# Optimization experiments

Hardware: AMD Instinct MI355X
Metric: run time of the kernel (lower is better)

## Reference

```python
import jax, jax.numpy as jnp
import numpy as np

NUM_USERS = 100000
NUM_ITEMS = 50000
HIDDEN = 64
NUM_LAYERS = 3
NUM_EDGES = 1200000
N = NUM_USERS + NUM_ITEMS


def setup_inputs() -> dict:
    key = jax.random.key(0)
    k_e, k_u, k_i, k_w, k_b = jax.random.split(key, 5)
    edge_index = jax.random.randint(k_e, (2, NUM_EDGES), 0, N, dtype=jnp.int32)
    users_emb = jax.random.normal(k_u, (NUM_USERS, HIDDEN), dtype=jnp.float32) * 0.01
    items_emb = jax.random.normal(k_i, (NUM_ITEMS, HIDDEN), dtype=jnp.float32) * 0.01
    # GCNConv linear weights (glorot-ish) and zero biases, stacked over layers
    scale = 1.0 / np.sqrt(HIDDEN)
    Ws = jax.random.uniform(k_w, (NUM_LAYERS, HIDDEN, HIDDEN), dtype=jnp.float32,
                            minval=-scale, maxval=scale)
    bs = jnp.zeros((NUM_LAYERS, HIDDEN), dtype=jnp.float32)
    return {"edge_index": edge_index, "users_emb": users_emb,
            "items_emb": items_emb, "Ws": Ws, "bs": bs}


def reference(edge_index, users_emb, items_emb, Ws, bs):
    # GraphSAGEModel.forward: concat user/item embeddings, run num_layers GCNConv
    # (PyG defaults: add self-loops, symmetric D^-1/2 A D^-1/2 normalization, bias).
    x = jnp.concatenate([users_emb, items_emb], axis=0)  # [N, H]

    self_loops = jnp.arange(N, dtype=edge_index.dtype)
    src = jnp.concatenate([edge_index[0], self_loops])  # [E+N]
    dst = jnp.concatenate([edge_index[1], self_loops])

    ones = jnp.ones(src.shape[0], dtype=x.dtype)
    deg = jax.ops.segment_sum(ones, dst, num_segments=N)  # in-degree incl self loop
    dinv = jnp.where(deg > 0, jax.lax.rsqrt(deg), 0.0)
    norm = dinv[src] * dinv[dst]  # [E+N], graph-constant across layers

    for l in range(NUM_LAYERS):
        h = x @ Ws[l]                       # linear transform [N, H]
        msg = h[src] * norm[:, None]        # gather + scale
        x = jax.ops.segment_sum(msg, dst, num_segments=N) + bs[l]
    return (x[:NUM_USERS], users_emb, x[NUM_USERS:], items_emb)
```

## Files before the change

### kernel.cpp

```cpp
#include <hip/hip_runtime.h>
#include <hip/hip_fp16.h>

#define NU 100000
#define NI 50000
#define NN 150000
#define HH 64
#define NE 1200000

#define SCAN_CHUNK 1024
#define NBLK ((NN + SCAN_CHUNK - 1) / SCAN_CHUNK)
#define AGG_BLOCKS (NN / 8)

__global__ __launch_bounds__(256) void k_rank(const int4* __restrict__ dst4,
                                              int* __restrict__ counts,
                                              int4* __restrict__ rank4,
                                              __half* __restrict__ pad0,
                                              __half* __restrict__ pad1,
                                              float* __restrict__ dinv,
                                              float* __restrict__ p1u) {
    if (blockIdx.x == 0 && threadIdx.x < 18) {
        if (threadIdx.x < 8)       ((int4*)pad0)[threadIdx.x] = make_int4(0, 0, 0, 0);
        else if (threadIdx.x < 16) ((int4*)pad1)[threadIdx.x - 8] = make_int4(0, 0, 0, 0);
        else if (threadIdx.x == 16) dinv[NN] = 0.f;
        else                        p1u[NN] = 0.f;
    }
    int t = blockIdx.x * blockDim.x + threadIdx.x;
    if (t >= NE / 8) return;
    int4 d0 = dst4[2 * t], d1 = dst4[2 * t + 1];
    int4 r0, r1;
    r0.x = atomicAdd(&counts[d0.x], 1);
    r0.y = atomicAdd(&counts[d0.y], 1);
    r0.z = atomicAdd(&counts[d0.z], 1);
    r0.w = atomicAdd(&counts[d0.w], 1);
    r1.x = atomicAdd(&counts[d1.x], 1);
    r1.y = atomicAdd(&counts[d1.y], 1);
    r1.z = atomicAdd(&counts[d1.z], 1);
    r1.w = atomicAdd(&counts[d1.w], 1);
    rank4[2 * t]     = r0;
    rank4[2 * t + 1] = r1;
}

__global__ __launch_bounds__(256) void k_scan(const int* __restrict__ counts,
                                              float* __restrict__ dinv,
                                              float* __restrict__ dinv2,
                                              int* __restrict__ row_ptr,
                                              unsigned int* __restrict__ state,
                                              const float* __restrict__ Wfull,
                                              const float* __restrict__ bfull,
                                              float* __restrict__ What,
                                              float* __restrict__ cvec) {
    __shared__ float smem[HH * HH];
    __shared__ int s_prefix;
    int t = threadIdx.x;
    int b = blockIdx.x;

    if (b == NBLK) {
        int r = t >> 2, j0 = (t & 3) * 16;
        const float* W0 = Wfull;
        const float* W1 = Wfull + HH * HH;
        const float* W2 = Wfull + 2 * HH * HH;
        float acc[16];
#pragma unroll
        for (int j = 0; j < 16; ++j) acc[j] = 0.f;
        for (int k = 0; k < HH; ++k) {
            float a = W1[r * HH + k];
            const float* bp = W2 + k * HH + j0;
#pragma unroll
            for (int j = 0; j < 16; ++j) acc[j] += a * bp[j];
        }
#pragma unroll
        for (int j = 0; j < 16; ++j) smem[r * HH + j0 + j] = acc[j];
        if (t < HH) {
            float s = 0.f;
            for (int k = 0; k < HH; ++k) s += bfull[HH + k] * W2[k * HH + t];
            cvec[HH + t] = s;
        }
        __syncthreads();
#pragma unroll
        for (int j = 0; j < 16; ++j) acc[j] = 0.f;
        for (int k = 0; k < HH; ++k) {
            float a = W0[r * HH + k];
            const float* bp = smem + k * HH + j0;
#pragma unroll
            for (int j = 0; j < 16; ++j) acc[j] += a * bp[j];
        }
#pragma unroll
        for (int j = 0; j < 16; ++j) What[r * HH + j0 + j] = acc[j];
        if (t < HH) {
            float s = 0.f;
            for (int k = 0; k < HH; ++k) s += bfull[k] * smem[k * HH + t];
            cvec[t] = s;
        }
        return;
    }

    int* sd = (int*)smem;
    int base = b * SCAN_CHUNK + t * 4;
    int c[4];
    if (base + 3 < NN) {
        int4 v = *(const int4*)(counts + base);
        c[0] = v.x; c[1] = v.y; c[2] = v.z; c[3] = v.w;
    } else {
#pragma unroll
        for (int i = 0; i < 4; ++i) c[i] = (base + i < NN) ? counts[base + i] : 0;
    }
#pragma unroll
    for (int i = 0; i < 4; ++i)
        if (base + i < NN) {
            dinv[base + i]  = rsqrtf((float)(c[i] + 1));
            dinv2[base + i] = 1.0f / (float)(c[i] + 1);
        }

    int tt = c[0] + c[1] + c[2] + c[3];
    sd[t] = tt; __syncthreads();
    for (int off = 1; off < 256; off <<= 1) {
        int x = (t >= off) ? sd[t - off] : 0;
        __syncthreads();
        sd[t] += x;
        __syncthreads();
    }

    if (t == 0) {
        unsigned int agg = (unsigned int)sd[255];
        if (b == 0) {
            __hip_atomic_store(&state[0], (2u << 30) | agg, __ATOMIC_RELEASE,
                               __HIP_MEMORY_SCOPE_AGENT);
            s_prefix = 0;
        } else {
            __hip_atomic_store(&state[b], (1u << 30) | agg, __ATOMIC_RELEASE,
                               __HIP_MEMORY_SCOPE_AGENT);
            unsigned int prefix = 0;
            int p = b - 1;
            while (true) {
                unsigned int s = __hip_atomic_load(&state[p], __ATOMIC_ACQUIRE,
                                                   __HIP_MEMORY_SCOPE_AGENT);
                unsigned int fl = s >> 30;
                if (fl == 0u) { __builtin_amdgcn_s_sleep(1); continue; }
                prefix += s & 0x3FFFFFFFu;
                if (fl == 2u) break;
                --p;
            }
            __hip_atomic_store(&state[b], (2u << 30) | (prefix + agg),
                               __ATOMIC_RELEASE, __HIP_MEMORY_SCOPE_AGENT);
            s_prefix = (int)prefix;
        }
    }
    __syncthreads();

    int off0 = s_prefix + (sd[t] - tt);
    int run = 0;
#pragma unroll
    for (int i = 0; i < 4; ++i) {
        if (base + i < NN) row_ptr[base + i] = off0 + run;
        run += c[i];
    }
    if (b == NBLK - 1 && t == 0) row_ptr[NN] = NE;
}

#define CONCAT_BLOCKS ((NN * 8 + 255) / 256)
#define FILL_BLOCKS   ((NE / 8 + 255) / 256)

__global__ __launch_bounds__(256) void k_concat_fill(
    const float4* __restrict__ users, const float4* __restrict__ items,
    const float* __restrict__ dinv, int4* __restrict__ xs4, float4* __restrict__ out,
    const int4* __restrict__ src4, const int4* __restrict__ dst4,
    const int4* __restrict__ rank4, const int* __restrict__ row_ptr,
    int* __restrict__ col) {
    if (blockIdx.x < CONCAT_BLOCKS) {
        int i = blockIdx.x * 256 + threadIdx.x;
        if (i >= NN * 8) return;
        const int UB8 = NU * 8;
        const int UB4 = NU * 16;
        float4 v0, v1;
        if (i < UB8) {
            v0 = users[2 * i];
            v1 = users[2 * i + 1];
            out[UB4 + 2 * i]     = v0;
            out[UB4 + 2 * i + 1] = v1;
        } else {
            int j = i - UB8;
            v0 = items[2 * j];
            v1 = items[2 * j + 1];
            out[2 * UB4 + NI * 16 + 2 * j]     = v0;
            out[2 * UB4 + NI * 16 + 2 * j + 1] = v1;
        }
        float dv = dinv[i >> 3];
        __half2 h[4];
        h[0] = __halves2half2(__float2half_rn(v0.x * dv), __float2half_rn(v0.y * dv));
        h[1] = __halves2half2(__float2half_rn(v0.z * dv), __float2half_rn(v0.w * dv));
        h[2] = __halves2half2(__float2half_rn(v1.x * dv), __float2half_rn(v1.y * dv));
        h[3] = __halves2half2(__float2half_rn(v1.z * dv), __float2half_rn(v1.w * dv));
        xs4[i] = *(int4*)h;
    } else {
        int t = (blockIdx.x - CONCAT_BLOCKS) * 256 + threadIdx.x;
        if (t >= NE / 8) return;
        int4 s0 = src4[2 * t],  s1 = src4[2 * t + 1];
        int4 d0 = dst4[2 * t],  d1 = dst4[2 * t + 1];
        int4 r0 = rank4[2 * t], r1 = rank4[2 * t + 1];
        int p0 = row_ptr[d0.x], p1 = row_ptr[d0.y], p2 = row_ptr[d0.z], p3 = row_ptr[d0.w];
        int p4 = row_ptr[d1.x], p5 = row_ptr[d1.y], p6 = row_ptr[d1.z], p7 = row_ptr[d1.w];
        col[p0 + r0.x] = s0.x;
        col[p1 + r0.y] = s0.y;
        col[p2 + r0.z] = s0.z;
        col[p3 + r0.w] = s0.w;
        col[p4 + r1.x] = s1.x;
        col[p5 + r1.y] = s1.y;
        col[p6 + r1.z] = s1.z;
        col[p7 + r1.w] = s1.w;
    }
}

template <int UMODE>
__global__ __launch_bounds__(256) void k_aggregate(
    const __half* __restrict__ x, __half* __restrict__ y,
    const float* __restrict__ scale,
    const int* __restrict__ row_ptr, const int* __restrict__ col,
    const float* __restrict__ dinv, const float* __restrict__ pin,
    float* __restrict__ uout, float* __restrict__ pout) {
    int lane = threadIdx.x & 63;
    int wave = blockIdx.x * 4 + (threadIdx.x >> 6);
    int na = wave * 2;
    if (na >= NN) return;
    int nb = na + 1;
    int o  = lane >> 3;
    int f8 = (lane & 7) << 3;

    float a[8], b[8];
#pragma unroll
    for (int j = 0; j < 8; ++j) { a[j] = 0.f; b[j] = 0.f; }
    float ua = 0.f, ub = 0.f;

#define GATHER(r, acc, uacc)                                               \
    {                                                                      \
        int4 raw = *(const int4*)(x + (size_t)(r) * HH + f8);              \
        if (UMODE) uacc += pin[r];                                         \
        __half2* hp = (__half2*)&raw;                                      \
        _Pragma("unroll")                                                  \
        for (int j = 0; j < 4; ++j) {                                      \
            float2 f = __half22float2(hp[j]);                              \
            acc[2 * j] += f.x; acc[2 * j + 1] += f.y;                      \
        }                                                                  \
    }

    int ea = row_ptr[na], enda = row_ptr[na + 1];
    int eb = enda,        endb = row_ptr[nb + 1];

    {
        int ia = ea + o - 1;
        int ib = eb + o - 1;
        int rA = (o == 0) ? na : ((ia < enda) ? col[ia] : NN);
        int rB = (o == 0) ? nb : ((ib < endb) ? col[ib] : NN);
        GATHER(rA, a, ua);
        GATHER(rB, b, ub);
        ea += 7; eb += 7;
    }
    while (ea < enda || eb < endb) {
        int iA = ea + o, iB = eb + o;
        int rA = (iA < enda) ? col[iA] : NN;
        int rB = (iB < endb) ? col[iB] : NN;
        GATHER(rA, a, ua);
        GATHER(rB, b, ub);
        ea += 8; eb += 8;
    }
#undef GATHER

#pragma unroll
    for (int j = 0; j < 8; ++j) {
        a[j] += __shfl_xor(a[j], 8);  b[j] += __shfl_xor(b[j], 8);
        a[j] += __shfl_xor(a[j], 16); b[j] += __shfl_xor(b[j], 16);
        a[j] += __shfl_xor(a[j], 32); b[j] += __shfl_xor(b[j], 32);
    }
    if (UMODE) {
        ua += __shfl_xor(ua, 8);  ub += __shfl_xor(ub, 8);
        ua += __shfl_xor(ua, 16); ub += __shfl_xor(ub, 16);
        ua += __shfl_xor(ua, 32); ub += __shfl_xor(ub, 32);
    }

    if (o < 2) {
        int   n  = (o == 0) ? na : nb;
        float dv = scale[n];
        __half2 h[4];
#pragma unroll
        for (int j = 0; j < 4; ++j) {
            float x0 = (o == 0) ? a[2 * j]     : b[2 * j];
            float x1 = (o == 0) ? a[2 * j + 1] : b[2 * j + 1];
            h[j] = __halves2half2(__float2half_rn(dv * x0), __float2half_rn(dv * x1));
        }
        *(int4*)(y + (size_t)n * HH + f8) = *(int4*)h;
    }
    if (UMODE && lane < 2) {
        int n = na + lane;
        float s = ((lane == 0) ? ua : ub) * 0.125f;
        float dvn = dinv[n];
        float u = dvn * s;
        uout[n] = u;
        if (UMODE == 1) pout[n] = dvn * u;
    }
}

#define GR 128
#define XSS 65
__global__ __launch_bounds__(256) void k_gemm_final(
    const __half* __restrict__ y, const float* __restrict__ W,
    const float* __restrict__ b2, const float* __restrict__ cvec,
    const float* __restrict__ u1, const float* __restrict__ u2,
    float* __restrict__ out_lo, float* __restrict__ out_hi) {
    __shared__ float xs[GR * XSS];
    __shared__ float ws[HH * HH];
    int t = threadIdx.x;
    int rowBase = blockIdx.x * GR;

    {
        const float4* W4 = (const float4*)W;
        float4* ws4 = (float4*)ws;
#pragma unroll
        for (int i = 0; i < 4; ++i) ws4[i * 256 + t] = W4[i * 256 + t];
    }
#pragma unroll
    for (int it = 0; it < 4; ++it) {
        int g = it * 256 + t;
        int r = g >> 3;
        int c0 = (g & 7) * 8;
        int row = rowBase + r;
        if (row < NN) {
            int4 raw = *(const int4*)(y + (size_t)row * HH + c0);
            __half2 h0 = *(__half2*)&raw.x, h1 = *(__half2*)&raw.y;
            __half2 h2 = *(__half2*)&raw.z, h3 = *(__half2*)&raw.w;
            float2 f0 = __half22float2(h0), f1 = __half22float2(h1);
            float2 f2 = __half22float2(h2), f3 = __half22float2(h3);
            float* dp = xs + r * XSS + c0;
            dp[0] = f0.x; dp[1] = f0.y; dp[2] = f1.x; dp[3] = f1.y;
            dp[4] = f2.x; dp[5] = f2.y; dp[6] = f3.x; dp[7] = f3.y;
        }
    }
    __syncthreads();

    int tx = t & 7;
    int ty = t >> 3;
    int j0 = tx * 8;
    int r0 = ty * 4;

    float acc[4][8];
#pragma unroll
    for (int i = 0; i < 4; ++i)
#pragma unroll
        for (int j = 0; j < 8; ++j) acc[i][j] = 0.f;

    for (int k = 0; k < HH; ++k) {
        float4 w0 = *(const float4*)(ws + k * HH + j0);
        float4 w1 = *(const float4*)(ws + k * HH + j0 + 4);
        float wv[8] = {w0.x, w0.y, w0.z, w0.w, w1.x, w1.y, w1.z, w1.w};
#pragma unroll
        for (int i = 0; i < 4; ++i) {
            float xv = xs[(r0 + i) * XSS + k];
#pragma unroll
            for (int j = 0; j < 8; ++j) acc[i][j] += xv * wv[j];
        }
    }

    float c0j[8], c1j[8], b2j[8];
#pragma unroll
    for (int j = 0; j < 8; ++j) {
        c0j[j] = cvec[j0 + j];
        c1j[j] = cvec[HH + j0 + j];
        b2j[j] = b2[j0 + j];
    }

#pragma unroll
    for (int i = 0; i < 4; ++i) {
        int r = rowBase + r0 + i;
        if (r >= NN) continue;
        float u2r = u2[r], u1r = u1[r];
        float base[8];
#pragma unroll
        for (int j = 0; j < 8; ++j) base[j] = u2r * c0j[j] + u1r * c1j[j] + b2j[j];
        float4 o0 = make_float4(acc[i][0] + base[0], acc[i][1] + base[1],
                                acc[i][2] + base[2], acc[i][3] + base[3]);
        float4 o1 = make_float4(acc[i][4] + base[4], acc[i][5] + base[5],
                                acc[i][6] + base[6], acc[i][7] + base[7]);
        float* d = (r < NU) ? (out_lo + (size_t)r * HH)
                            : (out_hi + (size_t)(r - NU) * HH);
        *(float4*)(d + j0) = o0;
        *(float4*)(d + j0 + 4) = o1;
    }
}

extern "C" void kernel_launch(void* const* d_in, const int* in_sizes, int n_in,
                              void* d_out, int out_size, void* d_ws, size_t ws_size,
                              hipStream_t stream) {
    const int*   edge  = (const int*)d_in[0];
    const int*   src   = edge;
    const int*   dst   = edge + NE;
    const float* users = (const float*)d_in[1];
    const float* items = (const float*)d_in[2];
    const float* Ws    = (const float*)d_in[3];
    const float* bs    = (const float*)d_in[4];
    float*       out   = (float*)d_out;

    char* w = (char*)d_ws;
    __half* Xs0     = (__half*)w; w += (size_t)(NN + 1) * HH * 2;
    __half* Xs1     = (__half*)w; w += (size_t)(NN + 1) * HH * 2;
    float*  dinv    = (float*)w;  w += (size_t)(NN + 1) * 4;
    float*  dinv2   = (float*)w;  w += (size_t)NN * 4;
    float*  u1      = (float*)w;  w += (size_t)NN * 4;
    float*  p1u     = (float*)w;  w += (size_t)(NN + 1) * 4;
    float*  u2      = (float*)w;  w += (size_t)NN * 4;
    float*  What    = (float*)w;  w += (size_t)HH * HH * 4;
    float*  cvec    = (float*)w;  w += (size_t)2 * HH * 4;
    unsigned int* state = (unsigned int*)w; w += 256 * 4;
    int*    counts  = (int*)w;    w += (size_t)NN * 4;
    int*    row_ptr = (int*)w;    w += (size_t)(NN + 1) * 4;
    w += 12;
    int*    col     = (int*)w;    w += (size_t)NE * 4;
    int*    rank    = (int*)w;    w += (size_t)NE * 4;
    (void)ws_size; (void)in_sizes; (void)n_in; (void)out_size;

    hipMemsetAsync(state, 0, (size_t)(256 + NN) * sizeof(int), stream);

    k_rank<<<(NE / 8 + 255) / 256, 256, 0, stream>>>(
        (const int4*)dst, counts, (int4*)rank,
        Xs0 + (size_t)NN * HH, Xs1 + (size_t)NN * HH, dinv, p1u);
    k_scan<<<NBLK + 1, 256, 0, stream>>>(counts, dinv, dinv2, row_ptr, state,
                                         Ws, bs, What, cvec);
    k_concat_fill<<<CONCAT_BLOCKS + FILL_BLOCKS, 256, 0, stream>>>(
        (const float4*)users, (const float4*)items, dinv, (int4*)Xs0, (float4*)out,
        (const int4*)src, (const int4*)dst, (const int4*)rank, row_ptr, col);

    k_aggregate<1><<<AGG_BLOCKS, 256, 0, stream>>>(
        Xs0, Xs1, dinv2, row_ptr, col, dinv, dinv, u1, p1u);
    k_aggregate<2><<<AGG_BLOCKS, 256, 0, stream>>>(
        Xs1, Xs0, dinv2, row_ptr, col, dinv, p1u, u2, nullptr);
    k_aggregate<0><<<AGG_BLOCKS, 256, 0, stream>>>(
        Xs0, Xs1, dinv, row_ptr, col, nullptr, nullptr, nullptr, nullptr);

    const int GEMM_BLOCKS = (NN + GR - 1) / GR;
    k_gemm_final<<<GEMM_BLOCKS, 256, 0, stream>>>(
        Xs1, What, bs + 2 * HH, cvec, u1, u2,
        out , out + (size_t)2 * NU * HH );
}
```

Before: 403.9 us.

## Move embedding concat into rank kernel, apply dinv in first aggregate, unroll gather

The fp16 conversion and output copy of the user/item embeddings now run inside the rank-counting kernel, so they no longer depend on dinv from the scan. The dinv scaling of source rows is instead applied in the first aggregation pass, where the per-row pin value is already being loaded. The fill kernel is left with only CSR column placement. The aggregation edge loop is also unrolled to issue two gathers per node per iteration, giving more memory-level parallelism at the cost of extra registers. Rounding changes slightly because x is quantized to half before the dinv multiply rather than after.

```diff
diff --git a/kernel.cpp b/kernel.cpp
--- a/kernel.cpp
+++ b/kernel.cpp
@@ -11,33 +11,52 @@
 #define NBLK ((NN + SCAN_CHUNK - 1) / SCAN_CHUNK)
 #define AGG_BLOCKS (NN / 8)
 
-__global__ __launch_bounds__(256) void k_rank(const int4* __restrict__ dst4,
-                                              int* __restrict__ counts,
-                                              int4* __restrict__ rank4,
-                                              __half* __restrict__ pad0,
-                                              __half* __restrict__ pad1,
-                                              float* __restrict__ dinv,
-                                              float* __restrict__ p1u) {
-    if (blockIdx.x == 0 && threadIdx.x < 18) {
-        if (threadIdx.x < 8)       ((int4*)pad0)[threadIdx.x] = make_int4(0, 0, 0, 0);
-        else if (threadIdx.x < 16) ((int4*)pad1)[threadIdx.x - 8] = make_int4(0, 0, 0, 0);
-        else if (threadIdx.x == 16) dinv[NN] = 0.f;
-        else                        p1u[NN] = 0.f;
-    }
-    int t = blockIdx.x * blockDim.x + threadIdx.x;
-    if (t >= NE / 8) return;
-    int4 d0 = dst4[2 * t], d1 = dst4[2 * t + 1];
-    int4 r0, r1;
-    r0.x = atomicAdd(&counts[d0.x], 1);
-    r0.y = atomicAdd(&counts[d0.y], 1);
-    r0.z = atomicAdd(&counts[d0.z], 1);
-    r0.w = atomicAdd(&counts[d0.w], 1);
-    r1.x = atomicAdd(&counts[d1.x], 1);
-    r1.y = atomicAdd(&counts[d1.y], 1);
-    r1.z = atomicAdd(&counts[d1.z], 1);
-    r1.w = atomicAdd(&counts[d1.w], 1);
-    rank4[2 * t]     = r0;
-    rank4[2 * t + 1] = r1;
+#define RANK_BLOCKS   ((NE / 8 + 255) / 256)
+#define CONCAT4_BLOCKS (NN * 16 / 256)
+#define FILL_BLOCKS   ((NE / 8 + 255) / 256)
+
+__global__ __launch_bounds__(256) void k_rank_concat(
+    const int4* __restrict__ dst4, int* __restrict__ counts, int4* __restrict__ rank4,
+    const float4* __restrict__ users, const float4* __restrict__ items,
+    __half2* __restrict__ xs, float4* __restrict__ out,
+    __half* __restrict__ pad0, __half* __restrict__ pad1,
+    float* __restrict__ dinv, float* __restrict__ p1u) {
+    if (blockIdx.x < RANK_BLOCKS) {
+        if (blockIdx.x == 0 && threadIdx.x < 18) {
+            if (threadIdx.x < 8)       ((int4*)pad0)[threadIdx.x] = make_int4(0, 0, 0, 0);
+            else if (threadIdx.x < 16) ((int4*)pad1)[threadIdx.x - 8] = make_int4(0, 0, 0, 0);
+            else if (threadIdx.x == 16) dinv[NN] = 0.f;
+            else                        p1u[NN] = 0.f;
+        }
+        int t = blockIdx.x * 256 + threadIdx.x;
+        if (t >= NE / 8) return;
+        int4 d0 = dst4[2 * t], d1 = dst4[2 * t + 1];
+        int4 r0, r1;
+        r0.x = atomicAdd(&counts[d0.x], 1);
+        r0.y = atomicAdd(&counts[d0.y], 1);
+        r0.z = atomicAdd(&counts[d0.z], 1);
+        r0.w = atomicAdd(&counts[d0.w], 1);
+        r1.x = atomicAdd(&counts[d1.x], 1);
+        r1.y = atomicAdd(&counts[d1.y], 1);
+        r1.z = atomicAdd(&counts[d1.z], 1);
+        r1.w = atomicAdd(&counts[d1.w], 1);
+        rank4[2 * t]     = r0;
+        rank4[2 * t + 1] = r1;
+    } else {
+        int i = (blockIdx.x - RANK_BLOCKS) * 256 + threadIdx.x;
+        const int UB = NU * 16;
+        float4 v;
+        if (i < UB) {
+            v = users[i];
+            out[UB + i] = v;
+        } else {
+            int j = i - UB;
+            v = items[j];
+            out[2 * UB + NI * 16 + j] = v;
+        }
+        xs[2 * i]     = __halves2half2(__float2half_rn(v.x), __float2half_rn(v.y));
+        xs[2 * i + 1] = __halves2half2(__float2half_rn(v.z), __float2half_rn(v.w));
+    }
 }
 
 __global__ __launch_bounds__(256) void k_scan(const int* __restrict__ counts,
@@ -157,57 +176,26 @@
     if (b == NBLK - 1 && t == 0) row_ptr[NN] = NE;
 }
 
-#define CONCAT_BLOCKS ((NN * 8 + 255) / 256)
-#define FILL_BLOCKS   ((NE / 8 + 255) / 256)
-
-__global__ __launch_bounds__(256) void k_concat_fill(
-    const float4* __restrict__ users, const float4* __restrict__ items,
-    const float* __restrict__ dinv, int4* __restrict__ xs4, float4* __restrict__ out,
-    const int4* __restrict__ src4, const int4* __restrict__ dst4,
-    const int4* __restrict__ rank4, const int* __restrict__ row_ptr,
-    int* __restrict__ col) {
-    if (blockIdx.x < CONCAT_BLOCKS) {
-        int i = blockIdx.x * 256 + threadIdx.x;
-        if (i >= NN * 8) return;
-        const int UB8 = NU * 8;
-        const int UB4 = NU * 16;
-        float4 v0, v1;
-        if (i < UB8) {
-            v0 = users[2 * i];
-            v1 = users[2 * i + 1];
-            out[UB4 + 2 * i]     = v0;
-            out[UB4 + 2 * i + 1] = v1;
-        } else {
-            int j = i - UB8;
-            v0 = items[2 * j];
-            v1 = items[2 * j + 1];
-            out[2 * UB4 + NI * 16 + 2 * j]     = v0;
-            out[2 * UB4 + NI * 16 + 2 * j + 1] = v1;
-        }
-        float dv = dinv[i >> 3];
-        __half2 h[4];
-        h[0] = __halves2half2(__float2half_rn(v0.x * dv), __float2half_rn(v0.y * dv));
-        h[1] = __halves2half2(__float2half_rn(v0.z * dv), __float2half_rn(v0.w * dv));
-        h[2] = __halves2half2(__float2half_rn(v1.x * dv), __float2half_rn(v1.y * dv));
-        h[3] = __halves2half2(__float2half_rn(v1.z * dv), __float2half_rn(v1.w * dv));
-        xs4[i] = *(int4*)h;
-    } else {
-        int t = (blockIdx.x - CONCAT_BLOCKS) * 256 + threadIdx.x;
-        if (t >= NE / 8) return;
-        int4 s0 = src4[2 * t],  s1 = src4[2 * t + 1];
-        int4 d0 = dst4[2 * t],  d1 = dst4[2 * t + 1];
-        int4 r0 = rank4[2 * t], r1 = rank4[2 * t + 1];
-        int p0 = row_ptr[d0.x], p1 = row_ptr[d0.y], p2 = row_ptr[d0.z], p3 = row_ptr[d0.w];
-        int p4 = row_ptr[d1.x], p5 = row_ptr[d1.y], p6 = row_ptr[d1.z], p7 = row_ptr[d1.w];
-        col[p0 + r0.x] = s0.x;
-        col[p1 + r0.y] = s0.y;
-        col[p2 + r0.z] = s0.z;
-        col[p3 + r0.w] = s0.w;
-        col[p4 + r1.x] = s1.x;
-        col[p5 + r1.y] = s1.y;
-        col[p6 + r1.z] = s1.z;
-        col[p7 + r1.w] = s1.w;
-    }
+__global__ __launch_bounds__(256) void k_fill(const int4* __restrict__ src4,
+                                              const int4* __restrict__ dst4,
+                                              const int4* __restrict__ rank4,
+                                              const int* __restrict__ row_ptr,
+                                              int* __restrict__ col) {
+    int t = blockIdx.x * 256 + threadIdx.x;
+    if (t >= NE / 8) return;
+    int4 s0 = src4[2 * t],  s1 = src4[2 * t + 1];
+    int4 d0 = dst4[2 * t],  d1 = dst4[2 * t + 1];
+    int4 r0 = rank4[2 * t], r1 = rank4[2 * t + 1];
+    int p0 = row_ptr[d0.x], p1 = row_ptr[d0.y], p2 = row_ptr[d0.z], p3 = row_ptr[d0.w];
+    int p4 = row_ptr[d1.x], p5 = row_ptr[d1.y], p6 = row_ptr[d1.z], p7 = row_ptr[d1.w];
+    col[p0 + r0.x] = s0.x;
+    col[p1 + r0.y] = s0.y;
+    col[p2 + r0.z] = s0.z;
+    col[p3 + r0.w] = s0.w;
+    col[p4 + r1.x] = s1.x;
+    col[p5 + r1.y] = s1.y;
+    col[p6 + r1.z] = s1.z;
+    col[p7 + r1.w] = s1.w;
 }
 
 template <int UMODE>
@@ -233,12 +221,14 @@
 #define GATHER(r, acc, uacc)                                               \
     {                                                                      \
         int4 raw = *(const int4*)(x + (size_t)(r) * HH + f8);              \
-        if (UMODE) uacc += pin[r];                                         \
+        float dr = 1.f;                                                    \
+        if (UMODE) { dr = pin[r]; uacc += dr; }                            \
         __half2* hp = (__half2*)&raw;                                      \
         _Pragma("unroll")                                                  \
         for (int j = 0; j < 4; ++j) {                                      \
             float2 f = __half22float2(hp[j]);                              \
-            acc[2 * j] += f.x; acc[2 * j + 1] += f.y;                      \
+            if (UMODE == 1) { acc[2 * j] += dr * f.x; acc[2 * j + 1] += dr * f.y; } \
+            else            { acc[2 * j] += f.x;      acc[2 * j + 1] += f.y; }      \
         }                                                                  \
     }
 
@@ -255,12 +245,17 @@
         ea += 7; eb += 7;
     }
     while (ea < enda || eb < endb) {
-        int iA = ea + o, iB = eb + o;
-        int rA = (iA < enda) ? col[iA] : NN;
-        int rB = (iB < endb) ? col[iB] : NN;
-        GATHER(rA, a, ua);
-        GATHER(rB, b, ub);
-        ea += 8; eb += 8;
+        int iA0 = ea + o,     iA1 = ea + 8 + o;
+        int iB0 = eb + o,     iB1 = eb + 8 + o;
+        int rA0 = (iA0 < enda) ? col[iA0] : NN;
+        int rA1 = (iA1 < enda) ? col[iA1] : NN;
+        int rB0 = (iB0 < endb) ? col[iB0] : NN;
+        int rB1 = (iB1 < endb) ? col[iB1] : NN;
+        GATHER(rA0, a, ua);
+        GATHER(rA1, a, ua);
+        GATHER(rB0, b, ub);
+        GATHER(rB1, b, ub);
+        ea += 16; eb += 16;
     }
 #undef GATHER
 
@@ -417,13 +412,13 @@
 
     hipMemsetAsync(state, 0, (size_t)(256 + NN) * sizeof(int), stream);
 
-    k_rank<<<(NE / 8 + 255) / 256, 256, 0, stream>>>(
+    k_rank_concat<<<RANK_BLOCKS + CONCAT4_BLOCKS, 256, 0, stream>>>(
         (const int4*)dst, counts, (int4*)rank,
+        (const float4*)users, (const float4*)items, (__half2*)Xs0, (float4*)out,
         Xs0 + (size_t)NN * HH, Xs1 + (size_t)NN * HH, dinv, p1u);
     k_scan<<<NBLK + 1, 256, 0, stream>>>(counts, dinv, dinv2, row_ptr, state,
                                          Ws, bs, What, cvec);
-    k_concat_fill<<<CONCAT_BLOCKS + FILL_BLOCKS, 256, 0, stream>>>(
-        (const float4*)users, (const float4*)items, dinv, (int4*)Xs0, (float4*)out,
+    k_fill<<<FILL_BLOCKS, 256, 0, stream>>>(
         (const int4*)src, (const int4*)dst, (const int4*)rank, row_ptr, col);
 
     k_aggregate<1><<<AGG_BLOCKS, 256, 0, stream>>>(
```

Result: no change. 403.0 us (-0.2%).
